# Optimization experiments

Hardware: AMD Instinct MI355X
Metric: run time of the kernel (lower is better)

Reference implementation:

```python
import jax, jax.numpy as jnp
import numpy as np
from jax import lax

D_MODEL = 768
BATCH = 16
SEQ = 2048
N_BLOCKS = D_MODEL // 3
LN_EPS = 1e-5


def setup_inputs() -> dict:
    key = jax.random.key(0)
    ks = jax.random.split(key, 4)
    scale = 1.0 / np.sqrt(D_MODEL)
    x = jax.random.normal(ks[0], (BATCH, SEQ, D_MODEL), dtype=jnp.float32)
    W_biv = jax.random.normal(ks[1], (D_MODEL, D_MODEL), dtype=jnp.float32) * scale
    b_biv = jnp.zeros((D_MODEL,), dtype=jnp.float32)
    W_decay = jax.random.normal(ks[2], (1, D_MODEL), dtype=jnp.float32) * scale
    b_decay = jnp.full((1,), 1.4, dtype=jnp.float32)  # nn.init.constant_(decay_proj.bias, 1.4)
    W_in = jax.random.normal(ks[3], (D_MODEL, D_MODEL), dtype=jnp.float32) * scale
    b_in = jnp.zeros((D_MODEL,), dtype=jnp.float32)
    ln_gamma = jnp.ones((D_MODEL,), dtype=jnp.float32)
    ln_beta = jnp.zeros((D_MODEL,), dtype=jnp.float32)
    return {"x": x, "W_biv": W_biv, "b_biv": b_biv, "W_decay": W_decay,
            "b_decay": b_decay, "W_in": W_in, "b_in": b_in,
            "ln_gamma": ln_gamma, "ln_beta": ln_beta}


def _quat_rotate_blocks(h_blocks, biv):
    """h_blocks, biv: (batch, n_blocks, 3) -> rotated (batch, n_blocks, 3)."""
    norm_b = jnp.maximum(jnp.linalg.norm(biv, axis=-1, keepdims=True), 1e-8)
    half = norm_b * 0.5
    w = jnp.cos(half)[..., 0]
    s = (jnp.sin(half) / norm_b)[..., 0]
    # note the original maps bivector components in reversed order
    qx = s * biv[..., 2]
    qy = -s * biv[..., 1]
    qz = s * biv[..., 0]
    vx, vy, vz = h_blocks[..., 0], h_blocks[..., 1], h_blocks[..., 2]
    tx = 2.0 * (qy * vz - qz * vy)
    ty = 2.0 * (qz * vx - qx * vz)
    tz = 2.0 * (qx * vy - qy * vx)
    rx = vx + w * tx + (qy * tz - qz * ty)
    ry = vy + w * ty + (qz * tx - qx * tz)
    rz = vz + w * tz + (qx * ty - qy * tx)
    return jnp.stack([rx, ry, rz], axis=-1)


def reference(x, W_biv, b_biv, W_decay, b_decay, W_in, b_in, ln_gamma, ln_beta):
    B, S, D = x.shape
    nb = D // 3
    # precompute all per-timestep projections as big GEMMs
    biv = (jnp.einsum('bsd,ed->bse', x, W_biv) + b_biv).reshape(B, S, nb, 3)
    decay = jax.nn.sigmoid(jnp.einsum('bsd,ed->bse', x, W_decay) + b_decay)  # (B,S,1)
    inj = jnp.einsum('bsd,ed->bse', x, W_in) + b_in  # (B,S,D)

    def step(h, t):
        biv_t, decay_t, inj_t = t
        rot = _quat_rotate_blocks(h.reshape(B, nb, 3), biv_t).reshape(B, D)
        h_next = decay_t * rot + inj_t
        return h_next, h_next

    xs = (jnp.moveaxis(biv, 1, 0), jnp.moveaxis(decay, 1, 0), jnp.moveaxis(inj, 1, 0))
    h0 = jnp.zeros((B, D), dtype=x.dtype)
    _, out = lax.scan(step, h0, xs)  # (S,B,D)
    out = jnp.moveaxis(out, 0, 1)  # (B,S,D)

    mean = jnp.mean(out, axis=-1, keepdims=True)
    var = jnp.mean(jnp.square(out - mean), axis=-1, keepdims=True)
    normed = (out - mean) * lax.rsqrt(var + LN_EPS) * ln_gamma + ln_beta
    return normed + x
```

## Files before the change

kernel.cpp:

```cpp
#include <hip/hip_runtime.h>
#include <stdint.h>

#define D_MODEL 768
#define BATCH   16
#define SEQ     2048
#define M_ROWS  (BATCH * SEQ)
#define LN_EPS  1e-5f

#define CHUNKS  64
#define CLEN    (SEQ / CHUNKS)
#define PFB     8

typedef __attribute__((ext_vector_type(4))) float        f32x4;
typedef __attribute__((ext_vector_type(8))) __bf16       bf16x8;
typedef __attribute__((ext_vector_type(2))) unsigned int u32x2;

__device__ __forceinline__ unsigned short f2bf(float f) {
    union { float f; uint32_t u; } v; v.f = f;
    uint32_t u = v.u;
    uint32_t r = (u + 0x7FFFu + ((u >> 16) & 1u)) >> 16;
    return (unsigned short)r;
}
__device__ __forceinline__ float bf2f(unsigned short u) {
    union { uint32_t u; float f; } v; v.u = (uint32_t)u << 16; return v.f;
}
__device__ __forceinline__ float bfx(u32x2 v, int k) {
    unsigned int w = (k & 2) ? v[1] : v[0];
    return bf2f((unsigned short)(w >> ((k & 1) * 16)));
}

__device__ __forceinline__ void gload_lds16(const void* g, void* l) {
    __builtin_amdgcn_global_load_lds(
        (const __attribute__((address_space(1))) unsigned int*)g,
        (__attribute__((address_space(3))) unsigned int*)l,
        16, 0, 0);
}

__global__ __launch_bounds__(256) void k_conv(
    const float* __restrict__ x, const float* __restrict__ Wd,
    const float* __restrict__ bd, unsigned short* __restrict__ xb,
    float* __restrict__ decay,
    const float* __restrict__ Wb, const float* __restrict__ Wi,
    unsigned short* __restrict__ Wdst)
{
    int blk = blockIdx.x;
    int i   = threadIdx.x;
    if (blk >= M_ROWS) {
        const int NW = D_MODEL * D_MODEL;
        int g = (blk - M_ROWS) * 256 + i;
        int base = g * 4;
        unsigned short* dst = Wdst + base;
        const float* src;
        if (base < NW) { src = Wb + base; }
        else           { src = Wi + (base - NW); }
        float4 v = *(const float4*)src;
        ushort4 o;
        o.x = f2bf(v.x); o.y = f2bf(v.y); o.z = f2bf(v.z); o.w = f2bf(v.w);
        *(ushort4*)dst = o;
        return;
    }
    int row = blk;
    const float* xr = x + (size_t)row * D_MODEL;
    float v0 = xr[i], v1 = xr[i + 256], v2 = xr[i + 512];
    unsigned short* xbr = xb + (size_t)row * D_MODEL;
    xbr[i] = f2bf(v0); xbr[i + 256] = f2bf(v1); xbr[i + 512] = f2bf(v2);

    float part = v0 * Wd[i] + v1 * Wd[i + 256] + v2 * Wd[i + 512];
    #pragma unroll
    for (int off = 32; off; off >>= 1) part += __shfl_down(part, off);
    __shared__ float wsum[4];
    int wid = i >> 6, lane = i & 63;
    if (lane == 0) wsum[wid] = part;
    __syncthreads();
    if (i == 0) {
        float s = wsum[0] + wsum[1] + wsum[2] + wsum[3] + bd[0];
        decay[row] = 1.f / (1.f + __expf(-s));
    }
}

#define GBM 256
#define GBN 256
#define GNBX 6
#define GNBY 128

__global__ __launch_bounds__(512, 2) void k_gemm_fused(
    const unsigned short* __restrict__ A,
    const unsigned short* __restrict__ Bw,
    const float* __restrict__ bias_biv, const float* __restrict__ bias_in,
    u32x2* __restrict__ bivq, u32x2* __restrict__ injq)
{
    extern __shared__ unsigned short LDSBUF[];
    unsigned short* LA = LDSBUF;
    unsigned short* LB = LDSBUF + 32768;

    int id  = blockIdx.x;
    int swz = (id & 7) * 96 + (id >> 3);
    int bxc = swz % GNBX, byr = swz / GNBX;
    int m0 = byr * GBM, n0 = bxc * GBN;

    int tid  = threadIdx.x;
    int wid  = tid >> 6, lane = tid & 63;
    int wm = wid >> 2, wn = wid & 3;
    int rl = lane & 15, kq = lane >> 4;
    int sl = kq ^ ((rl >> 1) & 3);
    int aoff = (wm * 128 + rl) * 32 + sl * 8;
    int boff = (wn * 64  + rl) * 32 + sl * 8;

    f32x4 acc[8][4] = {};
    bf16x8 bfv[4];

    #define STAGE_UNIT(DBUF, KT, H, RH) do {                                     \
        int idx = (RH) * 512 + tid;                                              \
        int row = idx >> 2;                                                      \
        int ss  = ((idx & 3) ^ ((idx >> 3) & 3)) * 8;      \
        gload_lds16(A  + (size_t)(m0 + row) * D_MODEL + (KT) * 64 + (H) * 32 + ss, \
                    LA + (DBUF) * 16384 + (H) * 8192 + idx * 8);                 \
        gload_lds16(Bw + (size_t)(n0 + row) * D_MODEL + (KT) * 64 + (H) * 32 + ss, \
                    LB + (DBUF) * 16384 + (H) * 8192 + idx * 8);                 \
    } while (0)

    #define SUBPHASE(D, H, MH, DOSTAGE, SKT, SH, SRH, WAITSTR) do {              \
        const unsigned short* pa = LA + (D) * 16384 + (H) * 8192 + aoff + (MH) * 2048; \
        const unsigned short* pb = LB + (D) * 16384 + (H) * 8192 + boff;         \
        bf16x8 af[4];                                                            \
        _Pragma("unroll")                                                        \
        for (int i = 0; i < 4; ++i) af[i] = *(const bf16x8*)(pa + i * 512);      \
        if ((MH) == 0) {                                                         \
            _Pragma("unroll")                                                    \
            for (int j = 0; j < 4; ++j) bfv[j] = *(const bf16x8*)(pb + j * 512); \
        }                                                                        \
        if (DOSTAGE) STAGE_UNIT((D) ^ 1, SKT, SH, SRH);                          \
        asm volatile(WAITSTR ::: "memory");                                      \
        asm volatile("s_barrier" ::: "memory");                                  \
        asm volatile("s_waitcnt lgkmcnt(0)" ::: "memory");                       \
        __builtin_amdgcn_sched_barrier(0);                                       \
        __builtin_amdgcn_s_setprio(1);                                           \
        _Pragma("unroll")                                                        \
        for (int i = 0; i < 4; ++i)                                              \
            _Pragma("unroll")                                                    \
            for (int j = 0; j < 4; ++j)                                          \
                acc[(MH) * 4 + i][j] = __builtin_amdgcn_mfma_f32_16x16x32_bf16(  \
                    af[i], bfv[j], acc[(MH) * 4 + i][j], 0, 0, 0);               \
        __builtin_amdgcn_s_setprio(0);                                           \
        asm volatile("s_barrier" ::: "memory");                                  \
    } while (0)

    STAGE_UNIT(0, 0, 0, 0);
    STAGE_UNIT(0, 0, 0, 1);
    STAGE_UNIT(0, 0, 1, 0);
    STAGE_UNIT(0, 0, 1, 1);
    asm volatile("s_waitcnt vmcnt(4)" ::: "memory");
    asm volatile("s_barrier" ::: "memory");

    for (int kt = 0; kt < 10; ++kt) {
        int D = kt & 1;
        SUBPHASE(D, 0, 0, true, kt + 1, 0, 0, "");
        SUBPHASE(D, 0, 1, true, kt + 1, 0, 1, "s_waitcnt vmcnt(4)");
        SUBPHASE(D, 1, 0, true, kt + 1, 1, 0, "");
        SUBPHASE(D, 1, 1, true, kt + 1, 1, 1, "s_waitcnt vmcnt(4)");
    }
    SUBPHASE(0, 0, 0, true, 11, 0, 0, "");
    SUBPHASE(0, 0, 1, true, 11, 0, 1, "s_waitcnt vmcnt(4)");
    SUBPHASE(0, 1, 0, true, 11, 1, 0, "");
    SUBPHASE(0, 1, 1, true, 11, 1, 1, "s_waitcnt vmcnt(4)");
    SUBPHASE(1, 0, 0, false, 0, 0, 0, "");
    SUBPHASE(1, 0, 1, false, 0, 0, 0, "s_waitcnt vmcnt(0)");
    SUBPHASE(1, 1, 0, false, 0, 0, 0, "");
    SUBPHASE(1, 1, 1, false, 0, 0, 0, "");

    #undef SUBPHASE
    #undef STAGE_UNIT

    u32x2* Cq; const float* bias; int nloc;
    if (n0 < D_MODEL) { Cq = bivq; bias = bias_biv; nloc = n0; }
    else              { Cq = injq; bias = bias_in;  nloc = n0 - D_MODEL; }
    int cl = lane & 15;
    int qbase = (m0 >> 2) + wm * 32 + (lane >> 4);
    #pragma unroll
    for (int j = 0; j < 4; ++j) {
        int col = nloc + wn * 64 + j * 16 + cl;
        float bs = bias[col];
        #pragma unroll
        for (int i = 0; i < 8; ++i) {
            f32x4 a = acc[i][j];
            unsigned int lo = (unsigned int)f2bf(a[0] + bs) | ((unsigned int)f2bf(a[1] + bs) << 16);
            unsigned int hi = (unsigned int)f2bf(a[2] + bs) | ((unsigned int)f2bf(a[3] + bs) << 16);
            u32x2 pk = {lo, hi};
            Cq[(size_t)(qbase + i * 4) * D_MODEL + col] = pk;
        }
    }
}

#define QSTEP_CORE(BX,BY,BZ, IX,IY,IZ, DD)                              \
    {   float n2   = (BX)*(BX) + (BY)*(BY) + (BZ)*(BZ);                 \
        float nrm  = fmaxf(__builtin_sqrtf(n2), 1e-8f);                 \
        float half = 0.5f * nrm;                                        \
        float w = __cosf(half);                                         \
        float s = __sinf(half) / nrm;                                   \
        float qx = s * (BZ), qy = -s * (BY), qz = s * (BX);             \
        float tx = 2.f * (qy * hz - qz * hy);                           \
        float ty = 2.f * (qz * hx - qx * hz);                           \
        float tz = 2.f * (qx * hy - qy * hx);                           \
        float rx = hx + w * tx + (qy * tz - qz * ty);                   \
        float ry = hy + w * ty + (qz * tx - qx * tz);                   \
        float rz = hz + w * tz + (qx * ty - qy * tx);                   \
        hx = fmaf((DD), rx, (IX));                                      \
        hy = fmaf((DD), ry, (IY));                                      \
        hz = fmaf((DD), rz, (IZ));                                      \
        float nQw = w * Qw - qx * Qx - qy * Qy - qz * Qz;               \
        float nQx = w * Qx + Qw * qx + (qy * Qz - qz * Qy);             \
        float nQy = w * Qy + Qw * qy + (qz * Qx - qx * Qz);             \
        float nQz = w * Qz + Qw * qz + (qx * Qy - qy * Qx);             \
        Qw = nQw; Qx = nQx; Qy = nQy; Qz = nQz;                         \
        S *= (DD);                                                      \
    }

#define QSTEP_H(BX,BY,BZ, IX,IY,IZ, DD)                                 \
    {   float n2   = (BX)*(BX) + (BY)*(BY) + (BZ)*(BZ);                 \
        float nrm  = fmaxf(__builtin_sqrtf(n2), 1e-8f);                 \
        float half = 0.5f * nrm;                                        \
        float w = __cosf(half);                                         \
        float s = __sinf(half) / nrm;                                   \
        float qx = s * (BZ), qy = -s * (BY), qz = s * (BX);             \
        float tx = 2.f * (qy * hz - qz * hy);                           \
        float ty = 2.f * (qz * hx - qx * hz);                           \
        float tz = 2.f * (qx * hy - qy * hx);                           \
        float rx = hx + w * tx + (qy * tz - qz * ty);                   \
        float ry = hy + w * ty + (qz * tx - qx * tz);                   \
        float rz = hz + w * tz + (qx * ty - qy * tx);                   \
        hx = fmaf((DD), rx, (IX));                                      \
        hy = fmaf((DD), ry, (IY));                                      \
        hz = fmaf((DD), rz, (IZ));                                      \
    }

__global__ __launch_bounds__(256) void k_scan_p1(
    const u32x2* __restrict__ bivq, const u32x2* __restrict__ injq,
    const float* __restrict__ decay,
    float* __restrict__ ops)
{
    int j = threadIdx.x;
    int c = blockIdx.x & (CHUNKS - 1);
    int b = blockIdx.x >> 6;
    size_t qrow = ((size_t)b * SEQ + (size_t)c * CLEN) >> 2;
    const u32x2* bv = bivq + qrow * D_MODEL + 3 * j;
    const u32x2* ij = injq + qrow * D_MODEL + 3 * j;
    const float* dk = decay + (size_t)b * SEQ + c * CLEN;

    u32x2 Ab0, Ab1, Ab2, Ai0, Ai1, Ai2; f32x4 Ad;
    u32x2 Bb0, Bb1, Bb2, Bi0, Bi1, Bi2; f32x4 Bd;

    #define LOADQ1(P, q)                                                  \
        P##b0 = bv[(size_t)(q) * D_MODEL + 0];                            \
        P##b1 = bv[(size_t)(q) * D_MODEL + 1];                            \
        P##b2 = bv[(size_t)(q) * D_MODEL + 2];                            \
        P##i0 = ij[(size_t)(q) * D_MODEL + 0];                            \
        P##i1 = ij[(size_t)(q) * D_MODEL + 1];                            \
        P##i2 = ij[(size_t)(q) * D_MODEL + 2];                            \
        P##d  = *(const f32x4*)(dk + (q) * 4);

    #define PROC41(P)                                                     \
        _Pragma("unroll")                                                 \
        for (int k = 0; k < 4; ++k) {                                     \
            float bx = bfx(P##b0, k), by = bfx(P##b1, k), bz = bfx(P##b2, k); \
            float ix = bfx(P##i0, k), iy = bfx(P##i1, k), iz = bfx(P##i2, k); \
            float d = P##d[k];                                            \
            QSTEP_CORE(bx, by, bz, ix, iy, iz, d)                         \
        }

    float hx = 0.f, hy = 0.f, hz = 0.f;
    float Qw = 1.f, Qx = 0.f, Qy = 0.f, Qz = 0.f, S = 1.f;

    LOADQ1(A, 0)
    LOADQ1(B, 1)
    #pragma unroll
    for (int q0 = 0; q0 < CLEN / 4; q0 += 2) {
        PROC41(A)
        if (q0 + 2 < CLEN / 4) { LOADQ1(A, q0 + 2) }
        PROC41(B)
        if (q0 + 3 < CLEN / 4) { LOADQ1(B, q0 + 3) }
    }
    #undef LOADQ1
    #undef PROC41

    float* op = ops + ((size_t)(b * CHUNKS + c) * 256 + j) * 8;
    f32x4 o0 = {Qw, Qx, Qy, Qz};
    f32x4 o1 = {S, hx, hy, hz};
    *(f32x4*)op = o0;
    *(f32x4*)(op + 4) = o1;
}

__global__ __launch_bounds__(64) void k_scan_p2(
    const float* __restrict__ ops, unsigned short* __restrict__ hsb)
{
    int gid = blockIdx.x * 64 + threadIdx.x;
    int j = gid & 255, b = gid >> 8;

    float q0[PFB], q1[PFB], q2[PFB], q3[PFB], sc[PFB], o0[PFB], o1[PFB], o2[PFB];
    #pragma unroll
    for (int p = 0; p < PFB; ++p) {
        const float* op = ops + ((size_t)(b * CHUNKS + p) * 256 + j) * 8;
        f32x4 a = *(const f32x4*)op, bb = *(const f32x4*)(op + 4);
        q0[p] = a[0]; q1[p] = a[1]; q2[p] = a[2]; q3[p] = a[3];
        sc[p] = bb[0]; o0[p] = bb[1]; o1[p] = bb[2]; o2[p] = bb[3];
    }
    float hx = 0.f, hy = 0.f, hz = 0.f;
    for (int c0 = 0; c0 < CHUNKS; c0 += PFB) {
        #pragma unroll
        for (int p = 0; p < PFB; ++p) {
            int c = c0 + p;
            unsigned short* h = hsb + ((size_t)(b * CHUNKS + c) * 256 + j) * 3;
            h[0] = f2bf(hx); h[1] = f2bf(hy); h[2] = f2bf(hz);
            float w = q0[p], qx = q1[p], qy = q2[p], qz = q3[p];
            float s = sc[p], bx = o0[p], by = o1[p], bz = o2[p];
            int cn = c + PFB;
            if (cn < CHUNKS) {
                const float* op = ops + ((size_t)(b * CHUNKS + cn) * 256 + j) * 8;
                f32x4 a = *(const f32x4*)op, bb = *(const f32x4*)(op + 4);
                q0[p] = a[0]; q1[p] = a[1]; q2[p] = a[2]; q3[p] = a[3];
                sc[p] = bb[0]; o0[p] = bb[1]; o1[p] = bb[2]; o2[p] = bb[3];
            }
            float tx = 2.f * (qy * hz - qz * hy);
            float ty = 2.f * (qz * hx - qx * hz);
            float tz = 2.f * (qx * hy - qy * hx);
            float rx = hx + w * tx + (qy * tz - qz * ty);
            float ry = hy + w * ty + (qz * tx - qx * tz);
            float rz = hz + w * tz + (qx * ty - qy * tx);
            hx = fmaf(s, rx, bx);
            hy = fmaf(s, ry, by);
            hz = fmaf(s, rz, bz);
        }
    }
}

__global__ __launch_bounds__(256) void k_scan_p3(
    const u32x2* __restrict__ bivq, const u32x2* __restrict__ injq,
    const float* __restrict__ decay, const unsigned short* __restrict__ hsb,
    const unsigned short* __restrict__ xb, const float* __restrict__ gamma,
    const float* __restrict__ beta, float* __restrict__ out)
{
    int blk = blockIdx.x;
    int c = blk & (CHUNKS - 1);
    int b = blk >> 6;
    int j = threadIdx.x;
    size_t row0 = (size_t)b * SEQ + (size_t)c * CLEN;
    size_t qrow = row0 >> 2;
    const u32x2* bv = bivq + qrow * D_MODEL + 3 * j;
    const u32x2* ij = injq + qrow * D_MODEL + 3 * j;
    const float* dk = decay + row0;
    const unsigned short* h0p = hsb + ((size_t)(b * CHUNKS + c) * 256 + j) * 3;
    float hx = bf2f(h0p[0]), hy = bf2f(h0p[1]), hz = bf2f(h0p[2]);

    __shared__ uint32_t       hxyS[16 * 256];
    __shared__ unsigned short hzS [16 * 256];

    int wid = j >> 6, lane = j & 63;
    const float4* g4 = (const float4*)(gamma + lane * 12);
    const float4* e4 = (const float4*)(beta  + lane * 12);
    float4 G0 = g4[0], G1 = g4[1], G2 = g4[2];
    float4 E0 = e4[0], E1 = e4[1], E2 = e4[2];
    const unsigned short* xbase = xb  + row0 * D_MODEL;
    float*                obase = out + row0 * D_MODEL;

    auto LN_HALF = [&](int H) {
        #pragma unroll
        for (int r = wid; r < 16; r += 4) {
            uint4   hv = *(const uint4*)  &hxyS[r * 256 + 4 * lane];
            ushort4 zv = *(const ushort4*)&hzS [r * 256 + 4 * lane];
            float h[12];
            h[0]  = bf2f((unsigned short)(hv.x & 0xFFFF)); h[1]  = bf2f((unsigned short)(hv.x >> 16)); h[2]  = bf2f(zv.x);
            h[3]  = bf2f((unsigned short)(hv.y & 0xFFFF)); h[4]  = bf2f((unsigned short)(hv.y >> 16)); h[5]  = bf2f(zv.y);
            h[6]  = bf2f((unsigned short)(hv.z & 0xFFFF)); h[7]  = bf2f((unsigned short)(hv.z >> 16)); h[8]  = bf2f(zv.z);
            h[9]  = bf2f((unsigned short)(hv.w & 0xFFFF)); h[10] = bf2f((unsigned short)(hv.w >> 16)); h[11] = bf2f(zv.w);
            float sp = 0.f, qp = 0.f;
            #pragma unroll
            for (int k = 0; k < 12; ++k) { sp += h[k]; qp += h[k] * h[k]; }
            #pragma unroll
            for (int off = 1; off < 64; off <<= 1) {
                sp += __shfl_xor(sp, off);
                qp += __shfl_xor(qp, off);
            }
            float mean = sp * (1.f / 768.f);
            float var  = qp * (1.f / 768.f) - mean * mean;
            float rstd = rsqrtf(var + LN_EPS);

            int t = H * 16 + r;
            const unsigned short* xr2 = xbase + (size_t)t * D_MODEL + lane * 12;
            float*                or2 = obase + (size_t)t * D_MODEL + lane * 12;
            ushort4 Xa = *(const ushort4*)(xr2 + 0);
            ushort4 Xb = *(const ushort4*)(xr2 + 4);
            ushort4 Xc = *(const ushort4*)(xr2 + 8);
            float4 O0, O1, O2;
            O0.x = (h[0]  - mean) * rstd * G0.x + E0.x + bf2f(Xa.x);
            O0.y = (h[1]  - mean) * rstd * G0.y + E0.y + bf2f(Xa.y);
            O0.z = (h[2]  - mean) * rstd * G0.z + E0.z + bf2f(Xa.z);
            O0.w = (h[3]  - mean) * rstd * G0.w + E0.w + bf2f(Xa.w);
            O1.x = (h[4]  - mean) * rstd * G1.x + E1.x + bf2f(Xb.x);
            O1.y = (h[5]  - mean) * rstd * G1.y + E1.y + bf2f(Xb.y);
            O1.z = (h[6]  - mean) * rstd * G1.z + E1.z + bf2f(Xb.z);
            O1.w = (h[7]  - mean) * rstd * G1.w + E1.w + bf2f(Xb.w);
            O2.x = (h[8]  - mean) * rstd * G2.x + E2.x + bf2f(Xc.x);
            O2.y = (h[9]  - mean) * rstd * G2.y + E2.y + bf2f(Xc.y);
            O2.z = (h[10] - mean) * rstd * G2.z + E2.z + bf2f(Xc.z);
            O2.w = (h[11] - mean) * rstd * G2.w + E2.w + bf2f(Xc.w);
            *(float4*)(or2 + 0) = O0;
            *(float4*)(or2 + 4) = O1;
            *(float4*)(or2 + 8) = O2;
        }
    };

    u32x2 Ab0, Ab1, Ab2, Ai0, Ai1, Ai2; f32x4 Ad;
    u32x2 Bb0, Bb1, Bb2, Bi0, Bi1, Bi2; f32x4 Bd;

    #define LOADQH(P, q)                                                  \
        P##b0 = bv[(size_t)(q) * D_MODEL + 0];                            \
        P##b1 = bv[(size_t)(q) * D_MODEL + 1];                            \
        P##b2 = bv[(size_t)(q) * D_MODEL + 2];                            \
        P##i0 = ij[(size_t)(q) * D_MODEL + 0];                            \
        P##i1 = ij[(size_t)(q) * D_MODEL + 1];                            \
        P##i2 = ij[(size_t)(q) * D_MODEL + 2];                            \
        P##d  = *(const f32x4*)(dk + (q) * 4);

    #define PROC4H(P, QBASE)                                              \
        _Pragma("unroll")                                                 \
        for (int k = 0; k < 4; ++k) {                                     \
            float bx = bfx(P##b0, k), by = bfx(P##b1, k), bz = bfx(P##b2, k); \
            float ix = bfx(P##i0, k), iy = bfx(P##i1, k), iz = bfx(P##i2, k); \
            float d = P##d[k];                                            \
            QSTEP_H(bx, by, bz, ix, iy, iz, d)                            \
            int tt = (((QBASE) * 4 + k) & 15);                            \
            hxyS[tt * 256 + j] = (uint32_t)f2bf(hx) | ((uint32_t)f2bf(hy) << 16); \
            hzS [tt * 256 + j] = f2bf(hz);                                \
        }

    LOADQH(A, 0)
    LOADQH(B, 1)
    PROC4H(A, 0) LOADQH(A, 2)
    PROC4H(B, 1) LOADQH(B, 3)
    PROC4H(A, 2) LOADQH(A, 4)
    PROC4H(B, 3) LOADQH(B, 5)
    __syncthreads();
    LN_HALF(0);
    __syncthreads();
    PROC4H(A, 4) LOADQH(A, 6)
    PROC4H(B, 5) LOADQH(B, 7)
    PROC4H(A, 6)
    PROC4H(B, 7)
    __syncthreads();
    LN_HALF(1);

    #undef LOADQH
    #undef PROC4H
}

extern "C" void kernel_launch(void* const* d_in, const int* in_sizes, int n_in,
                              void* d_out, int out_size, void* d_ws, size_t ws_size,
                              hipStream_t stream) {
    const float* x     = (const float*)d_in[0];
    const float* W_biv = (const float*)d_in[1];
    const float* b_biv = (const float*)d_in[2];
    const float* W_dec = (const float*)d_in[3];
    const float* b_dec = (const float*)d_in[4];
    const float* W_in  = (const float*)d_in[5];
    const float* b_in  = (const float*)d_in[6];
    const float* gamma = (const float*)d_in[7];
    const float* beta  = (const float*)d_in[8];
    float* out = (float*)d_out;

    char* ws = (char*)d_ws;
    unsigned short* xb    = (unsigned short*)(ws);
    unsigned short* Wcat  = (unsigned short*)(ws + 50331648);
    float*          decay = (float*)         (ws + 52690944);
    u32x2*          bivq  = (u32x2*)         (ws + 52822016);
    u32x2*          injq  = (u32x2*)         (ws + 103153664);
    float*          ops   = (float*)d_out;
    unsigned short* hsb   = (unsigned short*)(ws + 50331648);

    (void)in_sizes; (void)n_in; (void)out_size; (void)ws_size;

    hipFuncSetAttribute((const void*)k_gemm_fused,
                        hipFuncAttributeMaxDynamicSharedMemorySize, 131072);

    k_conv      <<<M_ROWS + 1152, 256, 0, stream>>>(x, W_dec, b_dec, xb, decay, W_biv, W_in, Wcat);
    k_gemm_fused<<<GNBX * GNBY, 512, 131072, stream>>>(xb, Wcat, b_biv, b_in, bivq, injq);
    k_scan_p1   <<<1024, 256, 0, stream>>>(bivq, injq, decay, ops);
    k_scan_p2   <<<64,   64,  0, stream>>>(ops, hsb);
    k_scan_p3   <<<1024, 256, 0, stream>>>(bivq, injq, decay, hsb, xb, gamma, beta, out);
}
```

Baseline: 207.0 us.

## Restructure fused GEMM to keep B panel in LDS and stream A from global

Result: slower. 310.5 us (+50.0%).

```diff
diff --git a/kernel.cpp b/kernel.cpp
--- a/kernel.cpp
+++ b/kernel.cpp
@@ -78,20 +78,19 @@
     }
 }
 
-#define GBM 256
-#define GBN 256
-#define GNBX 6
-#define GNBY 128
-
-__global__ __launch_bounds__(512, 2) void k_gemm_fused(
+#define GBM 1024
+#define GBN 64
+#define GNBX 24
+#define GNBY 32
+#define NKT 24
+
+__global__ __launch_bounds__(512) void k_gemm_fused(
     const unsigned short* __restrict__ A,
     const unsigned short* __restrict__ Bw,
     const float* __restrict__ bias_biv, const float* __restrict__ bias_in,
     u32x2* __restrict__ bivq, u32x2* __restrict__ injq)
 {
-    extern __shared__ unsigned short LDSBUF[];
-    unsigned short* LA = LDSBUF;
-    unsigned short* LB = LDSBUF + 32768;
+    extern __shared__ unsigned short LB[];
 
     int id  = blockIdx.x;
     int swz = (id & 7) * 96 + (id >> 3);
@@ -99,86 +98,64 @@
     int m0 = byr * GBM, n0 = bxc * GBN;
 
     int tid  = threadIdx.x;
-    int wid  = tid >> 6, lane = tid & 63;
-    int wm = wid >> 2, wn = wid & 3;
+    int w    = tid >> 6, lane = tid & 63;
     int rl = lane & 15, kq = lane >> 4;
     int sl = kq ^ ((rl >> 1) & 3);
-    int aoff = (wm * 128 + rl) * 32 + sl * 8;
-    int boff = (wn * 64  + rl) * 32 + sl * 8;
-
+
+    #pragma unroll
+    for (int p = 0; p < 12; ++p) {
+        int c    = p * 512 + tid;
+        int kt   = c >> 8;
+        int rem  = c & 255;
+        int col  = rem >> 2;
+        int slot = rem & 3;
+        int ssrc = slot ^ ((col >> 1) & 3);
+        gload_lds16(Bw + (size_t)(n0 + col) * D_MODEL + kt * 32 + ssrc * 8,
+                    LB + c * 8);
+    }
+    __syncthreads();
+
+    const unsigned short* Arow = A + (size_t)(m0 + w * 128 + rl) * D_MODEL + kq * 8;
     f32x4 acc[8][4] = {};
-    bf16x8 bfv[4];
-
-    #define STAGE_UNIT(DBUF, KT, H, RH) do {                                     \
-        int idx = (RH) * 512 + tid;                                              \
-        int row = idx >> 2;                                                      \
-        int ss  = ((idx & 3) ^ ((idx >> 3) & 3)) * 8;      \
-        gload_lds16(A  + (size_t)(m0 + row) * D_MODEL + (KT) * 64 + (H) * 32 + ss, \
-                    LA + (DBUF) * 16384 + (H) * 8192 + idx * 8);                 \
-        gload_lds16(Bw + (size_t)(n0 + row) * D_MODEL + (KT) * 64 + (H) * 32 + ss, \
-                    LB + (DBUF) * 16384 + (H) * 8192 + idx * 8);                 \
+    bf16x8 afA[8], afB[8];
+
+    #define LOADAF(RING, KT) do {                                                \
+        _Pragma("unroll")                                                        \
+        for (int i = 0; i < 8; ++i)                                              \
+            RING[i] = *(const bf16x8*)(Arow + (size_t)i * 16 * D_MODEL + (KT) * 32); \
     } while (0)
 
-    #define SUBPHASE(D, H, MH, DOSTAGE, SKT, SH, SRH, WAITSTR) do {              \
-        const unsigned short* pa = LA + (D) * 16384 + (H) * 8192 + aoff + (MH) * 2048; \
-        const unsigned short* pb = LB + (D) * 16384 + (H) * 8192 + boff;         \
-        bf16x8 af[4];                                                            \
+    #define KSTEP(RING, KT) do {                                                 \
+        bf16x8 bfv[4];                                                           \
+        const unsigned short* pb = LB + (KT) * 2048 + rl * 32 + sl * 8;          \
         _Pragma("unroll")                                                        \
-        for (int i = 0; i < 4; ++i) af[i] = *(const bf16x8*)(pa + i * 512);      \
-        if ((MH) == 0) {                                                         \
-            _Pragma("unroll")                                                    \
-            for (int j = 0; j < 4; ++j) bfv[j] = *(const bf16x8*)(pb + j * 512); \
-        }                                                                        \
-        if (DOSTAGE) STAGE_UNIT((D) ^ 1, SKT, SH, SRH);                          \
-        asm volatile(WAITSTR ::: "memory");                                      \
-        asm volatile("s_barrier" ::: "memory");                                  \
-        asm volatile("s_waitcnt lgkmcnt(0)" ::: "memory");                       \
-        __builtin_amdgcn_sched_barrier(0);                                       \
-        __builtin_amdgcn_s_setprio(1);                                           \
+        for (int j = 0; j < 4; ++j) bfv[j] = *(const bf16x8*)(pb + j * 512);     \
         _Pragma("unroll")                                                        \
-        for (int i = 0; i < 4; ++i)                                              \
+        for (int i = 0; i < 8; ++i)                                              \
             _Pragma("unroll")                                                    \
             for (int j = 0; j < 4; ++j)                                          \
-                acc[(MH) * 4 + i][j] = __builtin_amdgcn_mfma_f32_16x16x32_bf16(  \
-                    af[i], bfv[j], acc[(MH) * 4 + i][j], 0, 0, 0);               \
-        __builtin_amdgcn_s_setprio(0);                                           \
-        asm volatile("s_barrier" ::: "memory");                                  \
+                acc[i][j] = __builtin_amdgcn_mfma_f32_16x16x32_bf16(             \
+                    RING[i], bfv[j], acc[i][j], 0, 0, 0);                        \
+        if ((KT) + 2 < NKT) LOADAF(RING, (KT) + 2);                              \
     } while (0)
 
-    STAGE_UNIT(0, 0, 0, 0);
-    STAGE_UNIT(0, 0, 0, 1);
-    STAGE_UNIT(0, 0, 1, 0);
-    STAGE_UNIT(0, 0, 1, 1);
-    asm volatile("s_waitcnt vmcnt(4)" ::: "memory");
-    asm volatile("s_barrier" ::: "memory");
-
-    for (int kt = 0; kt < 10; ++kt) {
-        int D = kt & 1;
-        SUBPHASE(D, 0, 0, true, kt + 1, 0, 0, "");
-        SUBPHASE(D, 0, 1, true, kt + 1, 0, 1, "s_waitcnt vmcnt(4)");
-        SUBPHASE(D, 1, 0, true, kt + 1, 1, 0, "");
-        SUBPHASE(D, 1, 1, true, kt + 1, 1, 1, "s_waitcnt vmcnt(4)");
-    }
-    SUBPHASE(0, 0, 0, true, 11, 0, 0, "");
-    SUBPHASE(0, 0, 1, true, 11, 0, 1, "s_waitcnt vmcnt(4)");
-    SUBPHASE(0, 1, 0, true, 11, 1, 0, "");
-    SUBPHASE(0, 1, 1, true, 11, 1, 1, "s_waitcnt vmcnt(4)");
-    SUBPHASE(1, 0, 0, false, 0, 0, 0, "");
-    SUBPHASE(1, 0, 1, false, 0, 0, 0, "s_waitcnt vmcnt(0)");
-    SUBPHASE(1, 1, 0, false, 0, 0, 0, "");
-    SUBPHASE(1, 1, 1, false, 0, 0, 0, "");
-
-    #undef SUBPHASE
-    #undef STAGE_UNIT
+    LOADAF(afA, 0);
+    LOADAF(afB, 1);
+    #pragma unroll
+    for (int kt = 0; kt < NKT; kt += 2) {
+        KSTEP(afA, kt);
+        KSTEP(afB, kt + 1);
+    }
+    #undef KSTEP
+    #undef LOADAF
 
     u32x2* Cq; const float* bias; int nloc;
     if (n0 < D_MODEL) { Cq = bivq; bias = bias_biv; nloc = n0; }
     else              { Cq = injq; bias = bias_in;  nloc = n0 - D_MODEL; }
-    int cl = lane & 15;
-    int qbase = (m0 >> 2) + wm * 32 + (lane >> 4);
+    int qbase = (m0 >> 2) + w * 32 + kq;
     #pragma unroll
     for (int j = 0; j < 4; ++j) {
-        int col = nloc + wn * 64 + j * 16 + cl;
+        int col = nloc + j * 16 + rl;
         float bs = bias[col];
         #pragma unroll
         for (int i = 0; i < 8; ++i) {
@@ -478,10 +455,10 @@
     (void)in_sizes; (void)n_in; (void)out_size; (void)ws_size;
 
     hipFuncSetAttribute((const void*)k_gemm_fused,
-                        hipFuncAttributeMaxDynamicSharedMemorySize, 131072);
+                        hipFuncAttributeMaxDynamicSharedMemorySize, 98304);
 
     k_conv      <<<M_ROWS + 1152, 256, 0, stream>>>(x, W_dec, b_dec, xb, decay, W_biv, W_in, Wcat);
-    k_gemm_fused<<<GNBX * GNBY, 512, 131072, stream>>>(xb, Wcat, b_biv, b_in, bivq, injq);
+    k_gemm_fused<<<GNBX * GNBY, 512, 98304, stream>>>(xb, Wcat, b_biv, b_in, bivq, injq);
     k_scan_p1   <<<1024, 256, 0, stream>>>(bivq, injq, decay, ops);
     k_scan_p2   <<<64,   64,  0, stream>>>(ops, hsb);
     k_scan_p3   <<<1024, 256, 0, stream>>>(bivq, injq, decay, hsb, xb, gamma, beta, out);
```
